# Optimization experiments

Hardware: AMD Instinct MI355X
Metric: run time of the kernel (lower is better)

## Reference

```python
import jax, jax.numpy as jnp
import numpy as np

BN_EPS = 1e-5


def _bn_train(x, gamma, beta):
    # torch BatchNorm1d in training mode: normalize with batch mean and
    # biased batch variance.
    mu = jnp.mean(x, axis=0)
    var = jnp.var(x, axis=0)
    return (x - mu) * jax.lax.rsqrt(var + BN_EPS) * gamma + beta


def setup_inputs() -> dict:
    key = jax.random.key(0)
    ks = jax.random.split(key, 12)
    N, F_D, F_C, E, VOCAB, H = 16384, 26, 10, 16, 200000, 400
    D_IN = (F_D + F_C) * E  # 576
    return {
        "Xi_dense": jax.random.normal(ks[0], (N, F_D, 1), jnp.float32),
        "Xv": jax.random.uniform(ks[1], (N, F_D + F_C), jnp.float32),
        "Wd": jax.random.normal(ks[2], (F_D, E), jnp.float32) * 0.1,
        "bd": jax.random.normal(ks[3], (F_D, E), jnp.float32) * 0.1,
        "tables": jax.random.normal(ks[4], (F_C, VOCAB, E), jnp.float32) * 0.1,
        "W1": jax.random.normal(ks[5], (H, D_IN), jnp.float32) * 0.05,
        "b1": jax.random.normal(ks[6], (H,), jnp.float32) * 0.05,
        "g1": jnp.ones((H,), jnp.float32),
        "be1": jnp.zeros((H,), jnp.float32),
        "W2": jax.random.normal(ks[7], (H, H), jnp.float32) * 0.05,
        "b2": jax.random.normal(ks[8], (H,), jnp.float32) * 0.05,
        "g2": jnp.ones((H,), jnp.float32),
        "be2": jnp.zeros((H,), jnp.float32),
        "bias_vec": jax.random.normal(ks[9], (N,), jnp.float32),
        "Xi_cat": jax.random.randint(ks[10], (N, F_C, 1), 0, VOCAB, jnp.int32),
    }


def reference(Xi_dense, Xv, Wd, bd, tables, W1, b1, g1, be1,
              W2, b2, g2, be2, bias_vec, Xi_cat):
    N = Xi_dense.shape[0]
    # dense fields: per-field Linear(1, E) -> x * W + b, shape (N, 26, E)
    dense_emb = Xi_dense * Wd[None] + bd[None]  # (N,26,1)*(1,26,E) broadcast
    # categorical fields: per-field embedding lookup, shape (N, 10, E)
    cat_emb = jax.vmap(lambda tbl, idx: tbl[idx], in_axes=(0, 1), out_axes=1)(
        tables, Xi_cat[:, :, 0])
    # scale each field embedding by its Xv value
    all_emb = jnp.concatenate([dense_emb, cat_emb], axis=1) * Xv[:, :, None]  # (N,36,E)

    # fm first order: concat of all scaled field embeddings
    fm_first = all_emb.reshape(N, -1)  # (N, 576)
    # fm second order: 0.5 * ((sum)^2 - sum of squares)
    s = jnp.sum(all_emb, axis=1)                       # (N, E)
    fm_second = 0.5 * (s * s - jnp.sum(all_emb * all_emb, axis=1))  # (N, E)

    # deep part: Linear -> BatchNorm (train-mode stats) per hidden layer;
    # dropout p=0 -> identity.
    deep = fm_first
    deep = _bn_train(deep @ W1.T + b1, g1, be1)
    deep = _bn_train(deep @ W2.T + b2, g2, be2)

    total = (jnp.sum(fm_first, axis=1) + jnp.sum(fm_second, axis=1)
             + jnp.sum(deep, axis=1) + bias_vec)
    return total
```

## Files before the change

kernel.cpp:

```cpp
#include <hip/hip_runtime.h>

#define BN_EPS 1e-5f

typedef unsigned short u16;
typedef __attribute__((ext_vector_type(8))) short bf16x8;
typedef __attribute__((ext_vector_type(4))) float f32x4;

__device__ __forceinline__ u16 f2bf(float x) {
  union { float f; unsigned int u; } v; v.f = x;
  unsigned int r = v.u + 0x7fffu + ((v.u >> 16) & 1u);
  return (u16)(r >> 16);
}
__device__ __forceinline__ float bf2f(u16 h) {
  union { unsigned int u; float f; } v; v.u = ((unsigned int)h) << 16;
  return v.f;
}

__device__ __forceinline__ float wave_reduce_sum(float v) {
#pragma unroll
  for (int off = 1; off < 64; off <<= 1) v += __shfl_xor(v, off, 64);
  return v;
}

__device__ __forceinline__ void gload_lds16(const void* g, void* l) {
  __builtin_amdgcn_global_load_lds(
      (const __attribute__((address_space(1))) void*)g,
      (__attribute__((address_space(3))) void*)l, 16, 0, 0);
}

__global__ __launch_bounds__(256) void embed_prep(
    const float* __restrict__ Xi_dense, const float* __restrict__ Xv,
    const float* __restrict__ Wd, const float* __restrict__ bd,
    const float* __restrict__ tables, const int* __restrict__ Xi_cat,
    const float* __restrict__ bias_vec, const float* __restrict__ W1,
    u16* __restrict__ fm_first, float* __restrict__ partial,
    u16* __restrict__ W1h, float* __restrict__ statz) {
  const int t = threadIdx.x;
  if (blockIdx.x >= 512) {
    const int bb = blockIdx.x - 512;
    if (bb == 0) {
#pragma unroll
      for (int i = 0; i < 8; ++i) statz[i * 256 + t] = 0.f;
    }
    const int base = bb * 4096;
#pragma unroll
    for (int e = 0; e < 16; ++e) {
      const int idx = base + e * 256 + t;
      const int r = idx / 576;
      const int j = idx - r * 576;
      W1h[idx] = (r < 400) ? f2bf(W1[r * 576 + j]) : (u16)0;
    }
    return;
  }

  __shared__ float Xvs[32 * 37];
  __shared__ float Xds[32 * 27];
  __shared__ int Cis[32 * 11];
  __shared__ float Wds[416], Bds[416];
  const int n0 = blockIdx.x * 32;

  for (int i = t; i < 1152; i += 256) {
    const int r = i / 36;
    Xvs[r * 37 + (i - r * 36)] = Xv[n0 * 36 + i];
  }
  for (int i = t; i < 832; i += 256) {
    const int r = i / 26;
    Xds[r * 27 + (i - r * 26)] = Xi_dense[n0 * 26 + i];
  }
  for (int i = t; i < 320; i += 256) {
    const int r = i / 10;
    Cis[r * 11 + (i - r * 10)] = Xi_cat[n0 * 10 + i];
  }
  for (int i = t; i < 416; i += 256) {
    Wds[i] = Wd[i];
    Bds[i] = bd[i];
  }
  __syncthreads();

  const int r = t >> 3, q = t & 7;
  const int n = n0 + r;
  const int fbase = q >> 1, eh = (q & 1) * 8;
  float s8[8] = {}, q8[8] = {};
  float sum_all = 0.f;
  u16* frow = fm_first + (size_t)n * 576;

#pragma unroll
  for (int j = 0; j < 9; ++j) {
    const int f = fbase + 4 * j;
    const float xvv = Xvs[r * 37 + f];
    float val[8];
    if (f < 26) {
      const float xd = Xds[r * 27 + f];
      const float4 w0 = *(const float4*)&Wds[f * 16 + eh];
      const float4 w1 = *(const float4*)&Wds[f * 16 + eh + 4];
      const float4 b0 = *(const float4*)&Bds[f * 16 + eh];
      const float4 b1v = *(const float4*)&Bds[f * 16 + eh + 4];
      val[0] = fmaf(xd, w0.x, b0.x) * xvv;
      val[1] = fmaf(xd, w0.y, b0.y) * xvv;
      val[2] = fmaf(xd, w0.z, b0.z) * xvv;
      val[3] = fmaf(xd, w0.w, b0.w) * xvv;
      val[4] = fmaf(xd, w1.x, b1v.x) * xvv;
      val[5] = fmaf(xd, w1.y, b1v.y) * xvv;
      val[6] = fmaf(xd, w1.z, b1v.z) * xvv;
      val[7] = fmaf(xd, w1.w, b1v.w) * xvv;
    } else {
      const int fc = f - 26;
      const int row = Cis[r * 11 + fc];
      const float* tp =
          tables + ((size_t)fc * 200000 + (size_t)row) * 16 + eh;
      const float4 v0 = *(const float4*)tp;
      const float4 v1 = *(const float4*)(tp + 4);
      val[0] = v0.x * xvv;
      val[1] = v0.y * xvv;
      val[2] = v0.z * xvv;
      val[3] = v0.w * xvv;
      val[4] = v1.x * xvv;
      val[5] = v1.y * xvv;
      val[6] = v1.z * xvv;
      val[7] = v1.w * xvv;
    }
    bf16x8 o;
#pragma unroll
    for (int jj = 0; jj < 8; ++jj) {
      s8[jj] += val[jj];
      q8[jj] += val[jj] * val[jj];
      sum_all += val[jj];
      o[jj] = (short)f2bf(val[jj]);
    }
    *(bf16x8*)&frow[f * 16 + eh] = o;
  }

  float fm2h = 0.f;
#pragma unroll
  for (int jj = 0; jj < 8; ++jj) {
    float se = s8[jj] + __shfl_xor(s8[jj], 2, 64);
    se += __shfl_xor(se, 4, 64);
    float qe = q8[jj] + __shfl_xor(q8[jj], 2, 64);
    qe += __shfl_xor(qe, 4, 64);
    fm2h += se * se - qe;
  }
  const float fm2 = 0.5f * (fm2h + __shfl_xor(fm2h, 1, 64));
  float srow = sum_all + __shfl_xor(sum_all, 1, 64);
  srow += __shfl_xor(srow, 2, 64);
  srow += __shfl_xor(srow, 4, 64);
  if (q == 0) partial[n] = srow + fm2 + bias_vec[n];
}

__global__ __launch_bounds__(256) void gemm_bf16(
    const u16* __restrict__ A, int lda,
    const u16* __restrict__ W, int ldw,
    u16* __restrict__ Y, int ldc, int Ncap,
    float* __restrict__ aS, float* __restrict__ aQ, int K) {
  __shared__ u16 As[2][128 * 64];
  __shared__ u16 Bs[2][128 * 64];
  __shared__ float rS[2][4][2][16];
  __shared__ float rQ[2][4][2][16];

  const int t = threadIdx.x;
  const int bid = blockIdx.x;
  const int l = (bid & 7) * (gridDim.x >> 3) + (bid >> 3);
  const int bx = l >> 2, by = l & 3;
  const int bm = bx * 128, bn = by * 128;
  const int wid = t >> 6, lane = t & 63;
  const int wr = wid >> 1, wc = wid & 1;
  const int lr = lane & 15, hi = lane >> 4;
  const int sr = lane >> 3;
  const int sl = ((lane & 7) ^ sr) * 8;

  f32x4 acc[4][4] = {};

  auto STAGE = [&](int buf, int kt) {
#pragma unroll
    for (int i = 0; i < 8; ++i) {
      const int c = (wid & 1) * 8 + i;
      if (wid < 2)
        gload_lds16(&A[(size_t)(bm + c * 8 + sr) * lda + kt + sl],
                    &As[buf][c * 512]);
      else
        gload_lds16(&W[(size_t)(bn + c * 8 + sr) * ldw + kt + sl],
                    &Bs[buf][c * 512]);
    }
  };

  auto COMPUTE = [&](int buf) {
#pragma unroll
    for (int ks = 0; ks < 2; ++ks) {
      const int ps = ((ks * 4 + hi) ^ (lr & 7)) * 8;
      bf16x8 af[4], bfv[4];
#pragma unroll
      for (int mf = 0; mf < 4; ++mf)
        af[mf] = *(const bf16x8*)&As[buf][(wr * 64 + mf * 16 + lr) * 64 + ps];
#pragma unroll
      for (int nf = 0; nf < 4; ++nf)
        bfv[nf] =
            *(const bf16x8*)&Bs[buf][(wc * 64 + nf * 16 + lr) * 64 + ps];
      __builtin_amdgcn_s_setprio(1);
#pragma unroll
      for (int mf = 0; mf < 4; ++mf)
#pragma unroll
        for (int nf = 0; nf < 4; ++nf)
          acc[mf][nf] = __builtin_amdgcn_mfma_f32_16x16x32_bf16(
              af[mf], bfv[nf], acc[mf][nf], 0, 0, 0);
      __builtin_amdgcn_s_setprio(0);
    }
  };

  STAGE(0, 0);
  int cur = 0;
  for (int kt = 64; kt < K; kt += 64) {
    STAGE(cur ^ 1, kt);
    asm volatile("s_waitcnt vmcnt(8)" ::: "memory");
    __builtin_amdgcn_s_barrier();
    COMPUTE(cur);
    __builtin_amdgcn_s_barrier();
    cur ^= 1;
  }
  asm volatile("s_waitcnt vmcnt(0)" ::: "memory");
  __builtin_amdgcn_s_barrier();
  COMPUTE(cur);

  const int l4 = hi * 4;
  __syncthreads();
#pragma unroll
  for (int nf = 0; nf < 4; ++nf) {
    const int col = bn + wc * 64 + nf * 16 + lr;
    float s = 0.f, q = 0.f;
#pragma unroll
    for (int mf = 0; mf < 4; ++mf) {
#pragma unroll
      for (int r = 0; r < 4; ++r) {
        const int row = bm + wr * 64 + mf * 16 + l4 + r;
        const float v = acc[mf][nf][r];
        s += v;
        q += v * v;
        if (col < Ncap) Y[(size_t)row * ldc + col] = f2bf(v);
      }
    }
    s += __shfl_xor(s, 16, 64);
    s += __shfl_xor(s, 32, 64);
    q += __shfl_xor(q, 16, 64);
    q += __shfl_xor(q, 32, 64);
    if (lane < 16) {
      rS[wc][nf][wr][lr] = s;
      rQ[wc][nf][wr][lr] = q;
    }
  }
  __syncthreads();
  if (t < 128) {
    const int wcc = t >> 6, nff = (t >> 4) & 3, c = t & 15;
    atomicAdd(&aS[bn + t], rS[wcc][nff][0][c] + rS[wcc][nff][1][c]);
    atomicAdd(&aQ[bn + t], rQ[wcc][nff][0][c] + rQ[wcc][nff][1][c]);
  }
}

__global__ __launch_bounds__(256) void prep2(
    const float* __restrict__ aS1, const float* __restrict__ aQ1,
    const float* __restrict__ g1, const float* __restrict__ W2,
    u16* __restrict__ W2p) {
  const int c = blockIdx.x * 256 + threadIdx.x;
  const int row = c / 112;
  const int jc = (c - row * 112) * 4;
  ushort4 o = {0, 0, 0, 0};
  if (row < 400 && jc < 400) {
    const float4 S = *(const float4*)&aS1[jc];
    const float4 Q = *(const float4*)&aQ1[jc];
    const float4 G = *(const float4*)&g1[jc];
    const float4 w = *(const float4*)&W2[(size_t)row * 400 + jc];
    const float inv = 1.f / 16384.f;
    float mu, var, a;
    mu = S.x * inv; var = Q.x * inv - mu * mu;
    a = G.x * rsqrtf(var + BN_EPS); o.x = f2bf(w.x * a);
    mu = S.y * inv; var = Q.y * inv - mu * mu;
    a = G.y * rsqrtf(var + BN_EPS); o.y = f2bf(w.y * a);
    mu = S.z * inv; var = Q.z * inv - mu * mu;
    a = G.z * rsqrtf(var + BN_EPS); o.z = f2bf(w.z * a);
    mu = S.w * inv; var = Q.w * inv - mu * mu;
    a = G.w * rsqrtf(var + BN_EPS); o.w = f2bf(w.w * a);
  }
  *(ushort4*)&W2p[(size_t)row * 448 + jc] = o;
}

__device__ __forceinline__ void bn_affine4(const float* aS, const float* aQ,
                                           const float* g, const float* be,
                                           int j, float4& aa, float4& cc) {
  const float4 S = *(const float4*)&aS[j];
  const float4 Q = *(const float4*)&aQ[j];
  const float4 G = *(const float4*)&g[j];
  const float4 E = *(const float4*)&be[j];
  const float inv = 1.f / 16384.f;
  float mu, var;
  mu = S.x * inv; var = Q.x * inv - mu * mu;
  aa.x = G.x * rsqrtf(var + BN_EPS); cc.x = E.x - mu * aa.x;
  mu = S.y * inv; var = Q.y * inv - mu * mu;
  aa.y = G.y * rsqrtf(var + BN_EPS); cc.y = E.y - mu * aa.y;
  mu = S.z * inv; var = Q.z * inv - mu * mu;
  aa.z = G.z * rsqrtf(var + BN_EPS); cc.z = E.z - mu * aa.z;
  mu = S.w * inv; var = Q.w * inv - mu * mu;
  aa.w = G.w * rsqrtf(var + BN_EPS); cc.w = E.w - mu * aa.w;
}

__global__ __launch_bounds__(256) void final_kernel(
    const u16* __restrict__ Y2, const float* __restrict__ aS2,
    const float* __restrict__ aQ2, const float* __restrict__ g2,
    const float* __restrict__ be2, const float* __restrict__ partial,
    float* __restrict__ out) {
  const int t = threadIdx.x;
  const int lane = t & 63;
  const int wid = t >> 6;
  const int j0 = lane * 8;
  float ar[8], cr[8];
  if (j0 < 400) {
    float4 aa0, cc0, aa1, cc1;
    bn_affine4(aS2, aQ2, g2, be2, j0, aa0, cc0);
    bn_affine4(aS2, aQ2, g2, be2, j0 + 4, aa1, cc1);
    ar[0] = aa0.x; ar[1] = aa0.y; ar[2] = aa0.z; ar[3] = aa0.w;
    ar[4] = aa1.x; ar[5] = aa1.y; ar[6] = aa1.z; ar[7] = aa1.w;
    cr[0] = cc0.x; cr[1] = cc0.y; cr[2] = cc0.z; cr[3] = cc0.w;
    cr[4] = cc1.x; cr[5] = cc1.y; cr[6] = cc1.z; cr[7] = cc1.w;
  } else {
#pragma unroll
    for (int k = 0; k < 8; ++k) { ar[k] = 0.f; cr[k] = 0.f; }
  }
#pragma unroll
  for (int r = 0; r < 4; ++r) {
    const int n = blockIdx.x * 16 + wid * 4 + r;
    float acc = 0.f;
    if (j0 < 400) {
      const bf16x8 y = *(const bf16x8*)&Y2[(size_t)n * 400 + j0];
#pragma unroll
      for (int k = 0; k < 8; ++k)
        acc += fmaf(ar[k], bf2f((u16)y[k]), cr[k]);
    }
    acc = wave_reduce_sum(acc);
    if (lane == 0) out[n] = partial[n] + acc;
  }
}

extern "C" void kernel_launch(void* const* d_in, const int* in_sizes, int n_in,
                              void* d_out, int out_size, void* d_ws,
                              size_t ws_size, hipStream_t stream) {
  const float* Xi_dense = (const float*)d_in[0];
  const float* Xv = (const float*)d_in[1];
  const float* Wd = (const float*)d_in[2];
  const float* bd = (const float*)d_in[3];
  const float* tables = (const float*)d_in[4];
  const float* W1 = (const float*)d_in[5];
  const float* g1 = (const float*)d_in[7];
  const float* W2 = (const float*)d_in[9];
  const float* g2 = (const float*)d_in[11];
  const float* be2 = (const float*)d_in[12];
  const float* bias_vec = (const float*)d_in[13];
  const int* Xi_cat = (const int*)d_in[14];

  constexpr int N = 16384;
  constexpr int DIN = 576;
  constexpr int H = 400;
  constexpr int KP = 448;
  constexpr int WPAD = 512;

  u16* fm_first = (u16*)d_ws;
  u16* Y1h = fm_first + (size_t)N * DIN;
  u16* Y2h = Y1h + (size_t)N * KP;
  u16* W1h = Y2h + (size_t)N * H;
  u16* W2p = W1h + (size_t)WPAD * DIN;
  float* fptr = (float*)(W2p + (size_t)WPAD * KP);
  float* partial = fptr;
  float* aS1 = partial + N;
  float* aQ1 = aS1 + WPAD;
  float* aS2 = aQ1 + WPAD;
  float* aQ2 = aS2 + WPAD;

  embed_prep<<<512 + 72, 256, 0, stream>>>(Xi_dense, Xv, Wd, bd, tables,
                                           Xi_cat, bias_vec, W1, fm_first,
                                           partial, W1h, aS1);

  gemm_bf16<<<512, 256, 0, stream>>>(fm_first, DIN, W1h, DIN,
                                     Y1h, KP, KP, aS1, aQ1, DIN);

  prep2<<<224, 256, 0, stream>>>(aS1, aQ1, g1, W2, W2p);

  gemm_bf16<<<512, 256, 0, stream>>>(Y1h, KP, W2p, KP,
                                     Y2h, H, H, aS2, aQ2, KP);

  final_kernel<<<N / 16, 256, 0, stream>>>(Y2h, aS2, aQ2, g2, be2, partial,
                                           (float*)d_out);
}
```

Baseline: 57.88 us.

## Keep full-K weight tile resident in LDS and stream A fragments from global

Replaces the double-buffered 128x128 LDS-staged GEMM with a templated kernel that loads a 64-column, full-K slice of the weight matrix into swizzled LDS once. A fragments are then read directly from global memory into registers with a 6-deep prefetch ring, while B fragments are double-buffered from LDS. The aim is to remove the per-K-step barriers and A staging, and to raise occupancy with 896 blocks and two blocks per CU. In exchange, A reuse across columns is lower (7 column tiles instead of 4 re-read A), LDS use grows with K, and register pressure rises.

```diff
diff --git a/kernel.cpp b/kernel.cpp
--- a/kernel.cpp
+++ b/kernel.cpp
@@ -146,90 +146,86 @@
   if (q == 0) partial[n] = srow + fm2 + bias_vec[n];
 }
 
-__global__ __launch_bounds__(256) void gemm_bf16(
-    const u16* __restrict__ A, int lda,
-    const u16* __restrict__ W, int ldw,
+template <int K>
+__global__ __launch_bounds__(256, 2) void gemm_bres(
+    const u16* __restrict__ A,
+    const u16* __restrict__ W,
     u16* __restrict__ Y, int ldc, int Ncap,
-    float* __restrict__ aS, float* __restrict__ aQ, int K) {
-  __shared__ u16 As[2][128 * 64];
-  __shared__ u16 Bs[2][128 * 64];
-  __shared__ float rS[2][4][2][16];
-  __shared__ float rQ[2][4][2][16];
+    float* __restrict__ aS, float* __restrict__ aQ) {
+  constexpr int NI = K / 32;
+  constexpr int SL = K / 8;
+  __shared__ u16 Bs[64 * K];
+  __shared__ float rSQ[256];
 
   const int t = threadIdx.x;
   const int bid = blockIdx.x;
-  const int l = (bid & 7) * (gridDim.x >> 3) + (bid >> 3);
-  const int bx = l >> 2, by = l & 3;
-  const int bm = bx * 128, bn = by * 128;
+  const int l = (bid & 7) * 112 + (bid >> 3);
+  const int bx = l / 7, by = l - (l / 7) * 7;
+  const int bm = bx * 128, bn = by * 64;
   const int wid = t >> 6, lane = t & 63;
   const int wr = wid >> 1, wc = wid & 1;
   const int lr = lane & 15, hi = lane >> 4;
-  const int sr = lane >> 3;
-  const int sl = ((lane & 7) ^ sr) * 8;
-
-  f32x4 acc[4][4] = {};
-
-  auto STAGE = [&](int buf, int kt) {
-#pragma unroll
-    for (int i = 0; i < 8; ++i) {
-      const int c = (wid & 1) * 8 + i;
-      if (wid < 2)
-        gload_lds16(&A[(size_t)(bm + c * 8 + sr) * lda + kt + sl],
-                    &As[buf][c * 512]);
-      else
-        gload_lds16(&W[(size_t)(bn + c * 8 + sr) * ldw + kt + sl],
-                    &Bs[buf][c * 512]);
-    }
+
+#pragma unroll
+  for (int j = 0; j < (64 * SL) / 256; ++j) {
+    const int cid = j * 256 + t;
+    const int row = cid / SL;
+    const int slot = cid - row * SL;
+    gload_lds16(&W[(size_t)(bn + row) * K + ((slot ^ (row & 7)) << 3)],
+                &Bs[(size_t)(j * 256 + wid * 64) * 8]);
+  }
+  __syncthreads();
+
+  const u16* Ap = A + (size_t)(bm + wr * 64 + lr) * K + hi * 8;
+  bf16x8 af[6][4];
+  bf16x8 bfv[2][2];
+  f32x4 acc[4][2] = {};
+
+  auto LOADA = [&](bf16x8(&dst)[4], int kt) {
+#pragma unroll
+    for (int mf = 0; mf < 4; ++mf)
+      dst[mf] = *(const bf16x8*)&Ap[(size_t)(mf * 16) * K + kt];
   };
-
-  auto COMPUTE = [&](int buf) {
-#pragma unroll
-    for (int ks = 0; ks < 2; ++ks) {
-      const int ps = ((ks * 4 + hi) ^ (lr & 7)) * 8;
-      bf16x8 af[4], bfv[4];
-#pragma unroll
-      for (int mf = 0; mf < 4; ++mf)
-        af[mf] = *(const bf16x8*)&As[buf][(wr * 64 + mf * 16 + lr) * 64 + ps];
-#pragma unroll
-      for (int nf = 0; nf < 4; ++nf)
-        bfv[nf] =
-            *(const bf16x8*)&Bs[buf][(wc * 64 + nf * 16 + lr) * 64 + ps];
-      __builtin_amdgcn_s_setprio(1);
-#pragma unroll
-      for (int mf = 0; mf < 4; ++mf)
-#pragma unroll
-        for (int nf = 0; nf < 4; ++nf)
-          acc[mf][nf] = __builtin_amdgcn_mfma_f32_16x16x32_bf16(
-              af[mf], bfv[nf], acc[mf][nf], 0, 0, 0);
-      __builtin_amdgcn_s_setprio(0);
+  auto LOADB = [&](bf16x8(&dst)[2], int i) {
+    const int g = i * 4 + hi;
+#pragma unroll
+    for (int nf = 0; nf < 2; ++nf) {
+      const int row = wc * 32 + nf * 16 + lr;
+      dst[nf] =
+          *(const bf16x8*)&Bs[((size_t)row * SL + (g ^ (row & 7))) * 8];
     }
   };
 
-  STAGE(0, 0);
-  int cur = 0;
-  for (int kt = 64; kt < K; kt += 64) {
-    STAGE(cur ^ 1, kt);
-    asm volatile("s_waitcnt vmcnt(8)" ::: "memory");
-    __builtin_amdgcn_s_barrier();
-    COMPUTE(cur);
-    __builtin_amdgcn_s_barrier();
-    cur ^= 1;
-  }
-  asm volatile("s_waitcnt vmcnt(0)" ::: "memory");
-  __builtin_amdgcn_s_barrier();
-  COMPUTE(cur);
-
-  const int l4 = hi * 4;
-  __syncthreads();
-#pragma unroll
-  for (int nf = 0; nf < 4; ++nf) {
-    const int col = bn + wc * 64 + nf * 16 + lr;
+#pragma unroll
+  for (int i = 0; i < 6; ++i)
+    if (i < NI) LOADA(af[i], i * 32);
+  LOADB(bfv[0], 0);
+
+#pragma unroll
+  for (int i = 0; i < NI; ++i) {
+    if (i + 1 < NI) LOADB(bfv[(i + 1) & 1], i + 1);
+    __builtin_amdgcn_s_setprio(1);
+#pragma unroll
+    for (int mf = 0; mf < 4; ++mf)
+#pragma unroll
+      for (int nf = 0; nf < 2; ++nf)
+        acc[mf][nf] = __builtin_amdgcn_mfma_f32_16x16x32_bf16(
+            af[i % 6][mf], bfv[i & 1][nf], acc[mf][nf], 0, 0, 0);
+    __builtin_amdgcn_s_setprio(0);
+    if (i + 6 < NI) LOADA(af[i % 6], (i + 6) * 32);
+  }
+
+  float* rS = rSQ;
+  float* rQ = rSQ + 128;
+#pragma unroll
+  for (int nf = 0; nf < 2; ++nf) {
+    const int col = bn + wc * 32 + nf * 16 + lr;
     float s = 0.f, q = 0.f;
 #pragma unroll
     for (int mf = 0; mf < 4; ++mf) {
 #pragma unroll
       for (int r = 0; r < 4; ++r) {
-        const int row = bm + wr * 64 + mf * 16 + l4 + r;
+        const int row = bm + wr * 64 + mf * 16 + hi * 4 + r;
         const float v = acc[mf][nf][r];
         s += v;
         q += v * v;
@@ -241,15 +237,17 @@
     q += __shfl_xor(q, 16, 64);
     q += __shfl_xor(q, 32, 64);
     if (lane < 16) {
-      rS[wc][nf][wr][lr] = s;
-      rQ[wc][nf][wr][lr] = q;
+      rS[((wc * 2 + nf) * 2 + wr) * 16 + lr] = s;
+      rQ[((wc * 2 + nf) * 2 + wr) * 16 + lr] = q;
     }
   }
   __syncthreads();
-  if (t < 128) {
-    const int wcc = t >> 6, nff = (t >> 4) & 3, c = t & 15;
-    atomicAdd(&aS[bn + t], rS[wcc][nff][0][c] + rS[wcc][nff][1][c]);
-    atomicAdd(&aQ[bn + t], rQ[wcc][nff][0][c] + rQ[wcc][nff][1][c]);
+  if (t < 64) {
+    const int wcc = t >> 5, nff = (t >> 4) & 1, c = t & 15;
+    const int i0 = ((wcc * 2 + nff) * 2 + 0) * 16 + c;
+    const int i1 = ((wcc * 2 + nff) * 2 + 1) * 16 + c;
+    atomicAdd(&aS[bn + t], rS[i0] + rS[i1]);
+    atomicAdd(&aQ[bn + t], rQ[i0] + rQ[i1]);
   }
 }
 
@@ -374,13 +372,12 @@
                                            Xi_cat, bias_vec, W1, fm_first,
                                            partial, W1h, aS1);
 
-  gemm_bf16<<<512, 256, 0, stream>>>(fm_first, DIN, W1h, DIN,
-                                     Y1h, KP, KP, aS1, aQ1, DIN);
+  gemm_bres<DIN><<<896, 256, 0, stream>>>(fm_first, W1h, Y1h, KP, KP,
+                                          aS1, aQ1);
 
   prep2<<<224, 256, 0, stream>>>(aS1, aQ1, g1, W2, W2p);
 
-  gemm_bf16<<<512, 256, 0, stream>>>(Y1h, KP, W2p, KP,
-                                     Y2h, H, H, aS2, aQ2, KP);
+  gemm_bres<KP><<<896, 256, 0, stream>>>(Y1h, W2p, Y2h, H, H, aS2, aQ2);
 
   final_kernel<<<N / 16, 256, 0, stream>>>(Y2h, aS2, aQ2, g2, be2, partial,
                                            (float*)d_out);
```

Result: slower. 95.46 us (+64.9%).
